# Kernel optimization log

Measured on AMD Instinct MI355X. Metric: run time of the kernel, lower is better.

The kernel has to match this reference:

```python
import jax, jax.numpy as jnp
import numpy as np

HEADS = 8
DIM_HEAD = 64
EPS = 1.0
MAX_ITER = 3
SCALE = DIM_HEAD ** -0.5


def setup_inputs() -> dict:
    key = jax.random.key(0)
    k1, k2, k3, k4 = jax.random.split(key, 4)
    dim = 512
    inner = HEADS * DIM_HEAD
    x = jax.random.normal(k1, (8, 1024, dim), jnp.float32)
    W_qkv = jax.random.normal(k2, (dim, 3 * inner), jnp.float32) * (dim ** -0.5)
    W_out = jax.random.normal(k3, (inner, dim), jnp.float32) * (inner ** -0.5)
    b_out = jax.random.normal(k4, (dim,), jnp.float32) * 0.01
    return {"x": x, "W_qkv": W_qkv, "W_out": W_out, "b_out": b_out}


def _sinkhorn(C, eps, n_iter):
    # log-domain Sinkhorn with uniform marginals mu=1/n, nu=1/m; fixed n_iter.
    n, m = C.shape[-2], C.shape[-1]
    log_mu = -jnp.log(jnp.asarray(n, C.dtype))
    log_nu = -jnp.log(jnp.asarray(m, C.dtype))

    def M(u, v):
        return (-C + u[..., :, None] + v[..., None, :]) / eps

    u0 = jnp.zeros(C.shape[:-1], C.dtype)
    v0 = jnp.zeros(C.shape[:-2] + (m,), C.dtype)

    def body(carry, _):
        u, v = carry
        u = eps * (log_mu - jax.scipy.special.logsumexp(M(u, v), axis=-1)) + u
        v = eps * (log_nu - jax.scipy.special.logsumexp(M(u, v), axis=-2)) + v
        return (u, v), None

    (u, v), _ = jax.lax.scan(body, (u0, v0), None, length=n_iter)
    return jnp.exp(M(u, v))  # transport plan pi, rows sum ~ 1/n


def reference(x, W_qkv, W_out, b_out):
    b, n, _ = x.shape
    qkv = x @ W_qkv  # [b, n, 3*inner]
    q, k, v = jnp.split(qkv, 3, axis=-1)

    def heads(t):
        return t.reshape(b, n, HEADS, DIM_HEAD).transpose(0, 2, 1, 3)  # b h n d

    q, k, v = heads(q), heads(k), heads(v)
    dots = jnp.einsum('bhid,bhjd->bhij', q, k) * SCALE  # [b, h, n, n]
    attn = _sinkhorn(dots, EPS, MAX_ITER) * n  # rescale doubly-stochastic plan
    out = jnp.einsum('bhij,bhjd->bhid', attn, v)
    out = out.transpose(0, 2, 1, 3).reshape(b, n, HEADS * DIM_HEAD)
    return out @ W_out + b_out, attn
```

## Files before the change

### kernel.cpp

```cpp
#include <hip/hip_runtime.h>


#define MU (1.0f/1024.0f)
#define SCALE 0.125f

__global__ __launch_bounds__(256)
void k_gemm_qkv(const float* __restrict__ X, const float* __restrict__ W,
                float* __restrict__ Q) {
    __shared__ float aL[16][132];
    __shared__ float bL[16][132];
    const int n0 = blockIdx.x * 128;
    const int m0 = blockIdx.y * 128;
    const int t = threadIdx.x;
    const int tr = t >> 4, tc = t & 15;
    float acc[8][8] = {};
    for (int k0 = 0; k0 < 512; k0 += 16) {
#pragma unroll
        for (int q = 0; q < 2; ++q) {
            int p = t + 256 * q;
            int row = p >> 2, ks = (p & 3) * 4;
            float4 v = *reinterpret_cast<const float4*>(&X[(size_t)(m0 + row) * 512 + k0 + ks]);
            aL[ks + 0][row] = v.x; aL[ks + 1][row] = v.y;
            aL[ks + 2][row] = v.z; aL[ks + 3][row] = v.w;
        }
#pragma unroll
        for (int q = 0; q < 2; ++q) {
            int p = t + 256 * q;
            int kk = p >> 5, ns = (p & 31) * 4;
            *reinterpret_cast<float4*>(&bL[kk][ns]) =
                *reinterpret_cast<const float4*>(&W[(size_t)(k0 + kk) * 1536 + n0 + ns]);
        }
        __syncthreads();
#pragma unroll
        for (int kk = 0; kk < 16; ++kk) {
            float a8[8], b8[8];
#pragma unroll
            for (int r = 0; r < 8; ++r) a8[r] = aL[kk][tr * 8 + r];
#pragma unroll
            for (int c = 0; c < 8; ++c) b8[c] = bL[kk][tc * 8 + c];
#pragma unroll
            for (int r = 0; r < 8; ++r)
#pragma unroll
                for (int c = 0; c < 8; ++c)
                    acc[r][c] += a8[r] * b8[c];
        }
        __syncthreads();
    }
#pragma unroll
    for (int r = 0; r < 8; ++r)
#pragma unroll
        for (int c = 0; c < 8; c += 4) {
            float4 v = make_float4(acc[r][c], acc[r][c + 1], acc[r][c + 2], acc[r][c + 3]);
            *reinterpret_cast<float4*>(&Q[(size_t)(m0 + tr * 8 + r) * 1536 + n0 + tc * 8 + c]) = v;
        }
}

__global__ __launch_bounds__(256)
void k_qkT_exp(const float* __restrict__ QKV, float* __restrict__ E,
               float* __restrict__ r0) {
    __shared__ float qL[16][132];
    __shared__ float kL[16][132];
    __shared__ float rs[128];
    const int bi = blockIdx.x;
    const int s = bi >> 6, tile = bi & 63;
    const int i0 = (tile >> 3) * 128, j0 = (tile & 7) * 128;
    const int bb = s >> 3, h = s & 7;
    const int t = threadIdx.x, tr = t >> 4, tc = t & 15;
    const float* Qb = QKV + (size_t)bb * 1024 * 1536 + h * 64;
    const float* Kb = QKV + (size_t)bb * 1024 * 1536 + 512 + h * 64;
    float acc[8][8] = {};
    for (int d0 = 0; d0 < 64; d0 += 16) {
#pragma unroll
        for (int q = 0; q < 2; ++q) {
            int p = t + 256 * q;
            int row = p >> 2, ds = (p & 3) * 4;
            float4 v = *reinterpret_cast<const float4*>(&Qb[(size_t)(i0 + row) * 1536 + d0 + ds]);
            qL[ds + 0][row] = v.x; qL[ds + 1][row] = v.y;
            qL[ds + 2][row] = v.z; qL[ds + 3][row] = v.w;
            float4 w = *reinterpret_cast<const float4*>(&Kb[(size_t)(j0 + row) * 1536 + d0 + ds]);
            kL[ds + 0][row] = w.x; kL[ds + 1][row] = w.y;
            kL[ds + 2][row] = w.z; kL[ds + 3][row] = w.w;
        }
        __syncthreads();
#pragma unroll
        for (int d = 0; d < 16; ++d) {
            float a8[8], b8[8];
#pragma unroll
            for (int r = 0; r < 8; ++r) a8[r] = qL[d][tr * 8 + r];
#pragma unroll
            for (int c = 0; c < 8; ++c) b8[c] = kL[d][tc * 8 + c];
#pragma unroll
            for (int r = 0; r < 8; ++r)
#pragma unroll
                for (int c = 0; c < 8; ++c)
                    acc[r][c] += a8[r] * b8[c];
        }
        __syncthreads();
    }
    if (t < 128) rs[t] = 0.f;
    __syncthreads();
    float* Es = E + (size_t)s * 1024 * 1024;
#pragma unroll
    for (int r = 0; r < 8; ++r) {
        float e[8];
        float rsum = 0.f;
#pragma unroll
        for (int c = 0; c < 8; ++c) {
            e[c] = __expf(-acc[r][c] * SCALE);
            rsum += e[c];
        }
        size_t off = (size_t)(i0 + tr * 8 + r) * 1024 + j0 + tc * 8;
        *reinterpret_cast<float4*>(&Es[off])     = make_float4(e[0], e[1], e[2], e[3]);
        *reinterpret_cast<float4*>(&Es[off + 4]) = make_float4(e[4], e[5], e[6], e[7]);
        atomicAdd(&rs[tr * 8 + r], rsum);
    }
    __syncthreads();
    if (t < 128) atomicAdd(&r0[s * 1024 + i0 + t], rs[t]);
}

__global__ __launch_bounds__(256)
void k_colpass(const float* __restrict__ E, const float* __restrict__ ain,
               float* __restrict__ bout, int raw) {
    __shared__ float aL[1024];
    __shared__ float part[256];
    const int bi = blockIdx.x;
    const int s = bi >> 3, jc = (bi & 7) * 128;
    const int t = threadIdx.x;
    const float* as = ain + s * 1024;
    for (int i = t; i < 1024; i += 256)
        aL[i] = raw ? (MU / as[i]) : as[i];
    __syncthreads();
    const int j = jc + (t & 127);
    const int half = t >> 7;
    const int ib = half * 512;
    const float* Ep = E + (size_t)s * 1024 * 1024 + (size_t)ib * 1024 + j;
    float c = 0.f;
#pragma unroll 8
    for (int i = 0; i < 512; ++i)
        c += Ep[(size_t)i * 1024] * aL[ib + i];
    part[t] = c;
    __syncthreads();
    if (t < 128)
        bout[s * 1024 + j] = MU / (part[t] + part[t + 128]);
}

__global__ __launch_bounds__(256)
void k_rowpass(const float* __restrict__ E, const float* __restrict__ bin,
               float* __restrict__ aout) {
    __shared__ float bL[1024];
    const int bi = blockIdx.x;
    const int s = bi >> 6, i0 = (bi & 63) * 16;
    const int t = threadIdx.x;
    const float* bs = bin + s * 1024;
    for (int j = t; j < 1024; j += 256) bL[j] = bs[j];
    __syncthreads();
    const int w = t >> 6, l = t & 63;
#pragma unroll
    for (int rr = 0; rr < 4; ++rr) {
        const int i = i0 + w * 4 + rr;
        const float* Er = E + (size_t)s * 1024 * 1024 + (size_t)i * 1024;
        float sum = 0.f;
#pragma unroll
        for (int k = 0; k < 4; ++k) {
            int j4 = (l + k * 64) * 4;
            float4 e = *reinterpret_cast<const float4*>(&Er[j4]);
            sum += e.x * bL[j4] + e.y * bL[j4 + 1] + e.z * bL[j4 + 2] + e.w * bL[j4 + 3];
        }
#pragma unroll
        for (int off = 32; off; off >>= 1) sum += __shfl_xor(sum, off, 64);
        if (l == 0) aout[s * 1024 + i] = MU / sum;
    }
}

__global__ __launch_bounds__(256)
void k_finalize(float* __restrict__ E, const float* __restrict__ QKV,
                const float* __restrict__ a3, const float* __restrict__ b3,
                float* __restrict__ outp) {
    __shared__ float pT[64][132];
    __shared__ float vL[64][68];
    __shared__ float aLs[128];
    __shared__ float bn[1024];
    const int bi = blockIdx.x;
    const int s = bi >> 3, i0 = (bi & 7) * 128;
    const int bb = s >> 3, h = s & 7;
    const int t = threadIdx.x;
    for (int j = t; j < 1024; j += 256) bn[j] = 1024.f * b3[s * 1024 + j];
    if (t < 128) aLs[t] = a3[s * 1024 + i0 + t];
    __syncthreads();
    const float* Vb = QKV + (size_t)bb * 1024 * 1536 + 1024 + h * 64;
    float* Es = E + (size_t)s * 1024 * 1024;
    const int tr = t >> 4, tc = t & 15;
    const int rowi = t >> 1;
    const int jh = (t & 1) * 32;
    float acc[8][4] = {};
    for (int jc = 0; jc < 1024; jc += 64) {
#pragma unroll
        for (int q = 0; q < 4; ++q) {
            int p = t + 256 * q;
            int vr = p >> 4, vd = (p & 15) * 4;
            *reinterpret_cast<float4*>(&vL[vr][vd]) =
                *reinterpret_cast<const float4*>(&Vb[(size_t)(jc + vr) * 1536 + vd]);
        }
        float* Erow = &Es[(size_t)(i0 + rowi) * 1024 + jc + jh];
        const float ai = aLs[rowi];
#pragma unroll
        for (int q = 0; q < 8; ++q) {
            float4 e = *reinterpret_cast<float4*>(&Erow[q * 4]);
            int jj = jh + q * 4;
            float4 p4;
            p4.x = e.x * ai * bn[jc + jj];
            p4.y = e.y * ai * bn[jc + jj + 1];
            p4.z = e.z * ai * bn[jc + jj + 2];
            p4.w = e.w * ai * bn[jc + jj + 3];
            *reinterpret_cast<float4*>(&Erow[q * 4]) = p4;
            pT[jj][rowi] = p4.x; pT[jj + 1][rowi] = p4.y;
            pT[jj + 2][rowi] = p4.z; pT[jj + 3][rowi] = p4.w;
        }
        __syncthreads();
#pragma unroll
        for (int j = 0; j < 64; ++j) {
            float4 a0 = *reinterpret_cast<float4*>(&pT[j][tr * 8]);
            float4 a1 = *reinterpret_cast<float4*>(&pT[j][tr * 8 + 4]);
            float4 v4 = *reinterpret_cast<float4*>(&vL[j][tc * 4]);
            float a8[8] = {a0.x, a0.y, a0.z, a0.w, a1.x, a1.y, a1.z, a1.w};
#pragma unroll
            for (int r = 0; r < 8; ++r) {
                acc[r][0] += a8[r] * v4.x; acc[r][1] += a8[r] * v4.y;
                acc[r][2] += a8[r] * v4.z; acc[r][3] += a8[r] * v4.w;
            }
        }
        __syncthreads();
    }
#pragma unroll
    for (int r = 0; r < 8; ++r)
        *reinterpret_cast<float4*>(&outp[((size_t)s * 1024 + i0 + tr * 8 + r) * 64 + tc * 4]) =
            make_float4(acc[r][0], acc[r][1], acc[r][2], acc[r][3]);
}

__global__ __launch_bounds__(256)
void k_outproj(const float* __restrict__ outp, const float* __restrict__ Wo,
               const float* __restrict__ bo, float* __restrict__ Y) {
    __shared__ float aL[16][132];
    __shared__ float bL[16][132];
    const int n0 = blockIdx.x * 128;
    const int m0 = blockIdx.y * 128;
    const int t = threadIdx.x;
    const int tr = t >> 4, tc = t & 15;
    float acc[8][8] = {};
    for (int k0 = 0; k0 < 512; k0 += 16) {
        const int h = k0 >> 6, db = k0 & 63;
#pragma unroll
        for (int q = 0; q < 2; ++q) {
            int p = t + 256 * q;
            int row = p >> 2, ks = (p & 3) * 4;
            int gm = m0 + row;
            int bb = gm >> 10, ii = gm & 1023;
            float4 v = *reinterpret_cast<const float4*>(
                &outp[((size_t)(bb * 8 + h) * 1024 + ii) * 64 + db + ks]);
            aL[ks + 0][row] = v.x; aL[ks + 1][row] = v.y;
            aL[ks + 2][row] = v.z; aL[ks + 3][row] = v.w;
        }
#pragma unroll
        for (int q = 0; q < 2; ++q) {
            int p = t + 256 * q;
            int kk = p >> 5, ns = (p & 31) * 4;
            *reinterpret_cast<float4*>(&bL[kk][ns]) =
                *reinterpret_cast<const float4*>(&Wo[(size_t)(k0 + kk) * 512 + n0 + ns]);
        }
        __syncthreads();
#pragma unroll
        for (int kk = 0; kk < 16; ++kk) {
            float a8[8], b8[8];
#pragma unroll
            for (int r = 0; r < 8; ++r) a8[r] = aL[kk][tr * 8 + r];
#pragma unroll
            for (int c = 0; c < 8; ++c) b8[c] = bL[kk][tc * 8 + c];
#pragma unroll
            for (int r = 0; r < 8; ++r)
#pragma unroll
                for (int c = 0; c < 8; ++c)
                    acc[r][c] += a8[r] * b8[c];
        }
        __syncthreads();
    }
#pragma unroll
    for (int r = 0; r < 8; ++r)
#pragma unroll
        for (int c = 0; c < 8; c += 4) {
            float4 v = make_float4(acc[r][c] + bo[n0 + tc * 8 + c],
                                   acc[r][c + 1] + bo[n0 + tc * 8 + c + 1],
                                   acc[r][c + 2] + bo[n0 + tc * 8 + c + 2],
                                   acc[r][c + 3] + bo[n0 + tc * 8 + c + 3]);
            *reinterpret_cast<float4*>(&Y[(size_t)(m0 + tr * 8 + r) * 512 + n0 + tc * 8 + c]) = v;
        }
}

extern "C" void kernel_launch(void* const* d_in, const int* in_sizes, int n_in,
                              void* d_out, int out_size, void* d_ws, size_t ws_size,
                              hipStream_t stream) {
    (void)in_sizes; (void)n_in; (void)out_size; (void)ws_size;
    const float* x    = (const float*)d_in[0];
    const float* Wqkv = (const float*)d_in[1];
    const float* Wout = (const float*)d_in[2];
    const float* bout = (const float*)d_in[3];
    float* out2 = (float*)d_out;
    float* attn = out2 + (size_t)8192 * 512;

    float* ws   = (float*)d_ws;
    float* qkv  = ws;
    float* outp = qkv + (size_t)8192 * 1536;
    float* r0   = outp + (size_t)64 * 1024 * 64;
    float* abuf = r0 + 64 * 1024;
    float* bbuf = abuf + 64 * 1024;

    hipMemsetAsync(r0, 0, 64 * 1024 * sizeof(float), stream);
    k_gemm_qkv<<<dim3(12, 64), 256, 0, stream>>>(x, Wqkv, qkv);
    k_qkT_exp<<<4096, 256, 0, stream>>>(qkv, attn, r0);
    k_colpass<<<512, 256, 0, stream>>>(attn, r0, bbuf, 1);
    k_rowpass<<<4096, 256, 0, stream>>>(attn, bbuf, abuf);
    k_colpass<<<512, 256, 0, stream>>>(attn, abuf, bbuf, 0);
    k_rowpass<<<4096, 256, 0, stream>>>(attn, bbuf, abuf);
    k_colpass<<<512, 256, 0, stream>>>(attn, abuf, bbuf, 0);
    k_finalize<<<512, 256, 0, stream>>>(attn, qkv, abuf, bbuf, outp);
    k_outproj<<<dim3(4, 64), 256, 0, stream>>>(outp, Wout, bout, out2);
}
```

Measured before the change: 1.045 ms.

## Split column passes over row chunks and shrink finalize tiles for more parallelism

The column-sum pass now splits the 1024 rows into four chunks, so it launches four times as many blocks. Each block writes a partial column sum, and the consumers (rowpass and finalize) add the four partials and take the reciprocal. Finalize uses 64-row tiles with 32-column steps, doubling its grid, and uses nontemporal loads and stores for the attention-matrix rewrite. The aim is to raise occupancy on the bandwidth-bound passes that had only 512 blocks. The cost is redundant partial reductions in every consumer block and lower register reuse in the finalize matmul.

```diff
diff --git a/kernel.cpp b/kernel.cpp
--- a/kernel.cpp
+++ b/kernel.cpp
@@ -3,6 +3,8 @@
 
 #define MU (1.0f/1024.0f)
 #define SCALE 0.125f
+
+typedef float f32x4 __attribute__((ext_vector_type(4)));
 
 __global__ __launch_bounds__(256)
 void k_gemm_qkv(const float* __restrict__ X, const float* __restrict__ W,
@@ -120,39 +122,44 @@
 
 __global__ __launch_bounds__(256)
 void k_colpass(const float* __restrict__ E, const float* __restrict__ ain,
-               float* __restrict__ bout, int raw) {
-    __shared__ float aL[1024];
+               float* __restrict__ cpart, int raw) {
+    __shared__ float aL[256];
     __shared__ float part[256];
     const int bi = blockIdx.x;
-    const int s = bi >> 3, jc = (bi & 7) * 128;
-    const int t = threadIdx.x;
-    const float* as = ain + s * 1024;
-    for (int i = t; i < 1024; i += 256)
-        aL[i] = raw ? (MU / as[i]) : as[i];
+    const int s = bi >> 5;
+    const int rem = bi & 31;
+    const int jc = (rem >> 2) * 128;
+    const int ic = (rem & 3) * 256;
+    const int t = threadIdx.x;
+    const float* as = ain + s * 1024 + ic;
+    aL[t] = raw ? (MU / as[t]) : as[t];
     __syncthreads();
     const int j = jc + (t & 127);
     const int half = t >> 7;
-    const int ib = half * 512;
+    const int ib = ic + half * 128;
     const float* Ep = E + (size_t)s * 1024 * 1024 + (size_t)ib * 1024 + j;
     float c = 0.f;
 #pragma unroll 8
-    for (int i = 0; i < 512; ++i)
-        c += Ep[(size_t)i * 1024] * aL[ib + i];
+    for (int i = 0; i < 128; ++i)
+        c += Ep[(size_t)i * 1024] * aL[half * 128 + i];
     part[t] = c;
     __syncthreads();
     if (t < 128)
-        bout[s * 1024 + j] = MU / (part[t] + part[t + 128]);
-}
-
-__global__ __launch_bounds__(256)
-void k_rowpass(const float* __restrict__ E, const float* __restrict__ bin,
+        cpart[(size_t)(rem & 3) * 65536 + s * 1024 + j] = part[t] + part[t + 128];
+}
+
+__global__ __launch_bounds__(256)
+void k_rowpass(const float* __restrict__ E, const float* __restrict__ cpart,
                float* __restrict__ aout) {
     __shared__ float bL[1024];
     const int bi = blockIdx.x;
     const int s = bi >> 6, i0 = (bi & 63) * 16;
     const int t = threadIdx.x;
-    const float* bs = bin + s * 1024;
-    for (int j = t; j < 1024; j += 256) bL[j] = bs[j];
+    for (int j = t; j < 1024; j += 256) {
+        float c = cpart[s * 1024 + j] + cpart[65536 + s * 1024 + j]
+                + cpart[131072 + s * 1024 + j] + cpart[196608 + s * 1024 + j];
+        bL[j] = MU / c;
+    }
     __syncthreads();
     const int w = t >> 6, l = t & 63;
 #pragma unroll
@@ -174,66 +181,70 @@
 
 __global__ __launch_bounds__(256)
 void k_finalize(float* __restrict__ E, const float* __restrict__ QKV,
-                const float* __restrict__ a3, const float* __restrict__ b3,
+                const float* __restrict__ a3, const float* __restrict__ cpart,
                 float* __restrict__ outp) {
-    __shared__ float pT[64][132];
-    __shared__ float vL[64][68];
-    __shared__ float aLs[128];
+    __shared__ float pT[32][68];
+    __shared__ float vL[32][68];
+    __shared__ float aLs[64];
     __shared__ float bn[1024];
     const int bi = blockIdx.x;
-    const int s = bi >> 3, i0 = (bi & 7) * 128;
+    const int s = bi >> 4, i0 = (bi & 15) * 64;
     const int bb = s >> 3, h = s & 7;
     const int t = threadIdx.x;
-    for (int j = t; j < 1024; j += 256) bn[j] = 1024.f * b3[s * 1024 + j];
-    if (t < 128) aLs[t] = a3[s * 1024 + i0 + t];
+    for (int j = t; j < 1024; j += 256) {
+        float c = cpart[s * 1024 + j] + cpart[65536 + s * 1024 + j]
+                + cpart[131072 + s * 1024 + j] + cpart[196608 + s * 1024 + j];
+        bn[j] = 1024.f * (MU / c);
+    }
+    if (t < 64) aLs[t] = a3[s * 1024 + i0 + t];
     __syncthreads();
     const float* Vb = QKV + (size_t)bb * 1024 * 1536 + 1024 + h * 64;
     float* Es = E + (size_t)s * 1024 * 1024;
+    const int rowi = t >> 2;
+    const int jh = (t & 3) * 8;
     const int tr = t >> 4, tc = t & 15;
-    const int rowi = t >> 1;
-    const int jh = (t & 1) * 32;
-    float acc[8][4] = {};
-    for (int jc = 0; jc < 1024; jc += 64) {
-#pragma unroll
-        for (int q = 0; q < 4; ++q) {
+    float acc[4][4] = {};
+    for (int jc = 0; jc < 1024; jc += 32) {
+#pragma unroll
+        for (int q = 0; q < 2; ++q) {
             int p = t + 256 * q;
             int vr = p >> 4, vd = (p & 15) * 4;
             *reinterpret_cast<float4*>(&vL[vr][vd]) =
                 *reinterpret_cast<const float4*>(&Vb[(size_t)(jc + vr) * 1536 + vd]);
         }
-        float* Erow = &Es[(size_t)(i0 + rowi) * 1024 + jc + jh];
+        f32x4* Erow = reinterpret_cast<f32x4*>(&Es[(size_t)(i0 + rowi) * 1024 + jc + jh]);
         const float ai = aLs[rowi];
 #pragma unroll
-        for (int q = 0; q < 8; ++q) {
-            float4 e = *reinterpret_cast<float4*>(&Erow[q * 4]);
+        for (int q = 0; q < 2; ++q) {
+            f32x4 e = __builtin_nontemporal_load(Erow + q);
             int jj = jh + q * 4;
-            float4 p4;
+            f32x4 p4;
             p4.x = e.x * ai * bn[jc + jj];
             p4.y = e.y * ai * bn[jc + jj + 1];
             p4.z = e.z * ai * bn[jc + jj + 2];
             p4.w = e.w * ai * bn[jc + jj + 3];
-            *reinterpret_cast<float4*>(&Erow[q * 4]) = p4;
+            __builtin_nontemporal_store(p4, Erow + q);
             pT[jj][rowi] = p4.x; pT[jj + 1][rowi] = p4.y;
             pT[jj + 2][rowi] = p4.z; pT[jj + 3][rowi] = p4.w;
         }
         __syncthreads();
 #pragma unroll
-        for (int j = 0; j < 64; ++j) {
-            float4 a0 = *reinterpret_cast<float4*>(&pT[j][tr * 8]);
-            float4 a1 = *reinterpret_cast<float4*>(&pT[j][tr * 8 + 4]);
+        for (int j = 0; j < 32; ++j) {
+            float4 a4 = *reinterpret_cast<float4*>(&pT[j][tr * 4]);
             float4 v4 = *reinterpret_cast<float4*>(&vL[j][tc * 4]);
-            float a8[8] = {a0.x, a0.y, a0.z, a0.w, a1.x, a1.y, a1.z, a1.w};
-#pragma unroll
-            for (int r = 0; r < 8; ++r) {
-                acc[r][0] += a8[r] * v4.x; acc[r][1] += a8[r] * v4.y;
-                acc[r][2] += a8[r] * v4.z; acc[r][3] += a8[r] * v4.w;
-            }
-        }
-        __syncthreads();
-    }
-#pragma unroll
-    for (int r = 0; r < 8; ++r)
-        *reinterpret_cast<float4*>(&outp[((size_t)s * 1024 + i0 + tr * 8 + r) * 64 + tc * 4]) =
+            float a[4] = {a4.x, a4.y, a4.z, a4.w};
+            float v[4] = {v4.x, v4.y, v4.z, v4.w};
+#pragma unroll
+            for (int r = 0; r < 4; ++r)
+#pragma unroll
+                for (int c = 0; c < 4; ++c)
+                    acc[r][c] += a[r] * v[c];
+        }
+        __syncthreads();
+    }
+#pragma unroll
+    for (int r = 0; r < 4; ++r)
+        *reinterpret_cast<float4*>(&outp[((size_t)s * 1024 + i0 + tr * 4 + r) * 64 + tc * 4]) =
             make_float4(acc[r][0], acc[r][1], acc[r][2], acc[r][3]);
 }
 
@@ -306,21 +317,21 @@
     float* out2 = (float*)d_out;
     float* attn = out2 + (size_t)8192 * 512;
 
-    float* ws   = (float*)d_ws;
-    float* qkv  = ws;
-    float* outp = qkv + (size_t)8192 * 1536;
-    float* r0   = outp + (size_t)64 * 1024 * 64;
-    float* abuf = r0 + 64 * 1024;
-    float* bbuf = abuf + 64 * 1024;
+    float* ws    = (float*)d_ws;
+    float* qkv   = ws;
+    float* outp  = qkv + (size_t)8192 * 1536;
+    float* r0    = outp + (size_t)64 * 1024 * 64;
+    float* abuf  = r0 + 64 * 1024;
+    float* cpart = abuf + 64 * 1024;
 
     hipMemsetAsync(r0, 0, 64 * 1024 * sizeof(float), stream);
     k_gemm_qkv<<<dim3(12, 64), 256, 0, stream>>>(x, Wqkv, qkv);
     k_qkT_exp<<<4096, 256, 0, stream>>>(qkv, attn, r0);
-    k_colpass<<<512, 256, 0, stream>>>(attn, r0, bbuf, 1);
-    k_rowpass<<<4096, 256, 0, stream>>>(attn, bbuf, abuf);
-    k_colpass<<<512, 256, 0, stream>>>(attn, abuf, bbuf, 0);
-    k_rowpass<<<4096, 256, 0, stream>>>(attn, bbuf, abuf);
-    k_colpass<<<512, 256, 0, stream>>>(attn, abuf, bbuf, 0);
-    k_finalize<<<512, 256, 0, stream>>>(attn, qkv, abuf, bbuf, outp);
+    k_colpass<<<2048, 256, 0, stream>>>(attn, r0, cpart, 1);
+    k_rowpass<<<4096, 256, 0, stream>>>(attn, cpart, abuf);
+    k_colpass<<<2048, 256, 0, stream>>>(attn, abuf, cpart, 0);
+    k_rowpass<<<4096, 256, 0, stream>>>(attn, cpart, abuf);
+    k_colpass<<<2048, 256, 0, stream>>>(attn, abuf, cpart, 0);
+    k_finalize<<<1024, 256, 0, stream>>>(attn, qkv, abuf, cpart, outp);
     k_outproj<<<dim3(4, 64), 256, 0, stream>>>(outp, Wout, bout, out2);
 }
```

Result: no change. 1.030 ms (-1.4%).
